# Kernel optimization log

Measured on AMD Instinct MI355X. Metric: run time of the kernel, lower is better.

The kernel has to match this reference:

```python
import jax, jax.numpy as jnp
import numpy as np


def setup_inputs() -> dict:
    key = jax.random.key(0)
    k1, k2, k3, k4 = jax.random.split(key, 4)
    B, V, P, C, R, N, OUT = 8, 4096, 32, 32, 2, 16, 32  # N=(l_max+1)^2, l_max=3
    signal = jax.random.normal(k1, (B, V, C), dtype=jnp.float32)
    patches_idx = jax.random.randint(k2, (B, V, P), 0, V, dtype=jnp.int32)
    conv_kernel = jax.random.normal(k3, (B, V, P, R, N), dtype=jnp.float32)
    kernel_weights = jax.random.normal(k4, (OUT, C, R, N), dtype=jnp.float32) * 0.05
    biases = jnp.zeros((OUT,), dtype=jnp.float32)
    return {
        "signal": signal,
        "patches_idx": patches_idx,
        "conv_kernel": conv_kernel,
        "kernel_weights": kernel_weights,
        "biases": biases,
    }


def reference(signal, patches_idx, conv_kernel, kernel_weights, biases):
    # Gather per-vertex tree-neighbor patches (tf.gather_nd with batch idx):
    # signal [B,V,C], patches_idx [B,V,P] -> patches [B,V,P,C]
    patches = jax.vmap(lambda s, i: s[i])(signal, patches_idx)
    # Bilinear contraction with precomputed SH conv kernel: [B,V,P,R,N] x [B,V,P,C]
    y = jnp.einsum('bvprn,bvpc->bvcrn', conv_kernel, patches)
    # Learned weights contraction: [OUT,C,R,N] x [B,V,C,R,N] -> [B,V,OUT]
    y = jnp.einsum('ijrn,bvjrn->bvi', kernel_weights, y)
    y = y + biases
    return jax.nn.relu(y)
```

## Files before the change

kernel.cpp:

```cpp
#include <hip/hip_runtime.h>


typedef __attribute__((ext_vector_type(8))) short bf16x8;
typedef __attribute__((ext_vector_type(4))) short short4v;
typedef __attribute__((ext_vector_type(16))) float f32x16;
typedef __attribute__((ext_vector_type(4))) float f32x4;
typedef __attribute__((ext_vector_type(4))) int int4v;

#define KSTR 36

__device__ __forceinline__ unsigned short f2bf_rne(float f) {
    union { float f; unsigned int u; } x;
    x.f = f;
    unsigned int u = x.u;
    return (unsigned short)((u + 0x7fffu + ((u >> 16) & 1u)) >> 16);
}
__device__ __forceinline__ unsigned short f2bf_rh(float f) {
    union { float f; unsigned int u; } x;
    x.f = f;
    return (unsigned short)((x.u + 0x8000u) >> 16);
}

__global__ __launch_bounds__(256) void prep_kernel(
        const float* __restrict__ W, const float* __restrict__ sig,
        unsigned short* __restrict__ Wf, unsigned short* __restrict__ sigbf) {
    int tid = blockIdx.x * 256 + threadIdx.x;
    if (tid < 32768) {
        int j = tid & 7;
        int l = (tid >> 3) & 63;
        int pair = tid >> 9;
        int s = pair >> 1;
        int t = pair & 1;
        int i = 16 * t + (l & 15);
        int crn = 32 * s + 8 * (l >> 4) + j;
        Wf[tid] = f2bf_rne(W[i * 1024 + crn]);
    } else {
        int e = (tid - 32768) * 8;
        if (e < 8 * 4096 * 32) {
            f32x4 a = *(const f32x4*)(sig + e);
            f32x4 b = *(const f32x4*)(sig + e + 4);
            bf16x8 v;
            v[0] = (short)f2bf_rne(a[0]); v[1] = (short)f2bf_rne(a[1]);
            v[2] = (short)f2bf_rne(a[2]); v[3] = (short)f2bf_rne(a[3]);
            v[4] = (short)f2bf_rne(b[0]); v[5] = (short)f2bf_rne(b[1]);
            v[6] = (short)f2bf_rne(b[2]); v[7] = (short)f2bf_rne(b[3]);
            *(bf16x8*)(sigbf + e) = v;
        }
    }
}

__global__ __launch_bounds__(256) void fused_kernel(
        const unsigned short* __restrict__ sigbf, const int* __restrict__ pidx,
        const float* __restrict__ ck, const unsigned short* __restrict__ Wf,
        const float* __restrict__ bias, float* __restrict__ out) {
    __shared__ __align__(16) unsigned short T_lds[16 * 1032];
    __shared__ __align__(16) unsigned short K_lds[4 * 32 * KSTR];
    __shared__ __align__(16) int idx_lds[512];
    const int tid = threadIdx.x;
    const int l = tid & 63;
    const int w = tid >> 6;
    const int m0 = blockIdx.x * 16;
    const int b = m0 >> 12;
    const int cc = l & 31;
    const int g = l >> 5;
    const unsigned short* sgb = sigbf + (size_t)b * (4096 * 32);
    unsigned short* kl = K_lds + w * 32 * KSTR;

    f32x4 kreg[4][4];
    #pragma unroll
    for (int q = 0; q < 4; ++q) {
        const f32x4* kp = (const f32x4*)(ck + (size_t)(m0 + w * 4 + q) * 1024);
        #pragma unroll
        for (int t = 0; t < 4; ++t) kreg[q][t] = kp[t * 64 + l];
    }
    {
        const int2* src = (const int2*)(pidx + (size_t)m0 * 32);
        ((int2*)idx_lds)[tid] = src[tid];
    }
    __syncthreads();

    auto issue_gathers = [&](int q, unsigned short (&gq)[16]) {
        const int base = (w * 4 + q) * 32;
        int4v ia = *(const int4v*)(idx_lds + base + 8 * g);
        int4v ib = *(const int4v*)(idx_lds + base + 8 * g + 4);
        int4v ic = *(const int4v*)(idx_lds + base + 16 + 8 * g);
        int4v id = *(const int4v*)(idx_lds + base + 16 + 8 * g + 4);
        #pragma unroll
        for (int j = 0; j < 4; ++j) {
            gq[j]      = sgb[ia[j] * 32 + cc];
            gq[4 + j]  = sgb[ib[j] * 32 + cc];
            gq[8 + j]  = sgb[ic[j] * 32 + cc];
            gq[12 + j] = sgb[id[j] * 32 + cc];
        }
    };

    auto compute_q = [&](int q, const unsigned short (&gq)[16], const f32x4 (&kq)[4]) {
        #pragma unroll
        for (int t = 0; t < 4; ++t) {
            union { f32x4 f; unsigned int u[4]; } x;
            x.f = kq[t];
            short4v v = { (short)(x.u[0] >> 16), (short)(x.u[1] >> 16),
                          (short)(x.u[2] >> 16), (short)(x.u[3] >> 16) };
            *(short4v*)(kl + (t * 8 + (l >> 3)) * KSTR + 4 * (l & 7)) = v;
        }
        f32x16 acc = {};
        #pragma unroll
        for (int half = 0; half < 2; ++half) {
            bf16x8 af, bfr;
            #pragma unroll
            for (int j = 0; j < 8; ++j) {
                af[j]  = (short)gq[half * 8 + j];
                bfr[j] = (short)kl[(half * 16 + 8 * g + j) * KSTR + cc];
            }
            acc = __builtin_amdgcn_mfma_f32_32x32x16_bf16(af, bfr, acc, 0, 0, 0);
        }
        const int bvl = w * 4 + q;
        unsigned short* trow = T_lds + bvl * 1032 + cc + g * 128;
        #pragma unroll
        for (int r = 0; r < 16; ++r) {
            trow[((r & 3) + 8 * (r >> 2)) * 32] = f2bf_rh(acc[r]);
        }
    };

    unsigned short g0[16], g1[16];
    issue_gathers(0, g0);
    issue_gathers(1, g1);
    compute_q(0, g0, kreg[0]); issue_gathers(2, g0);
    compute_q(1, g1, kreg[1]); issue_gathers(3, g1);
    compute_q(2, g0, kreg[2]);
    compute_q(3, g1, kreg[3]);
    __syncthreads();

    f32x4 acc0 = {}, acc1 = {};
    const int lg = l >> 4;
    const int ln = l & 15;
    #pragma unroll
    for (int si = 0; si < 8; ++si) {
        const int s = 8 * w + si;
        const bf16x8 af = *(const bf16x8*)(T_lds + ln * 1032 + s * 32 + 8 * lg);
        const bf16x8* wrow = (const bf16x8*)(Wf + (size_t)(s * 2) * 512);
        const bf16x8 b0 = wrow[l];
        const bf16x8 b1 = wrow[64 + l];
        acc0 = __builtin_amdgcn_mfma_f32_16x16x32_bf16(af, b0, acc0, 0, 0, 0);
        acc1 = __builtin_amdgcn_mfma_f32_16x16x32_bf16(af, b1, acc1, 0, 0, 0);
    }
    __syncthreads();

    float* red = (float*)T_lds;
    {
        f32x4* rp = (f32x4*)(red + w * 512);
        rp[l]      = acc0;
        rp[64 + l] = acc1;
    }
    __syncthreads();

    #pragma unroll
    for (int o0 = 0; o0 < 2; ++o0) {
        const int o = o0 * 256 + tid;
        float sum = red[o] + red[512 + o] + red[1024 + o] + red[1536 + o];
        const int t  = o >> 8;
        const int ll = (o >> 2) & 63;
        const int r  = o & 3;
        const int bv = ((ll >> 4) << 2) + r;
        const int i  = 16 * t + (ll & 15);
        sum += bias[i];
        out[(size_t)(m0 + bv) * 32 + i] = sum > 0.f ? sum : 0.f;
    }
}

extern "C" void kernel_launch(void* const* d_in, const int* in_sizes, int n_in,
                              void* d_out, int out_size, void* d_ws, size_t ws_size,
                              hipStream_t stream) {
    const float* sig  = (const float*)d_in[0];
    const int*   pidx = (const int*)d_in[1];
    const float* ck   = (const float*)d_in[2];
    const float* W    = (const float*)d_in[3];
    const float* bias = (const float*)d_in[4];
    float* out = (float*)d_out;
    unsigned short* Wf    = (unsigned short*)d_ws;
    unsigned short* sigbf = Wf + 32768;

    prep_kernel<<<640, 256, 0, stream>>>(W, sig, Wf, sigbf);
    fused_kernel<<<2048, 256, 0, stream>>>(sigbf, pidx, ck, Wf, bias, out);
}
```

Before: 40.86 us.

## Drop bf16 prep kernel; convert signal and weights inline in fused kernel

Removes the separate prep kernel that converted the weights and the signal to bf16. The fused kernel now gathers fp32 signal values and reads fp32 weights directly, converting both to bf16 in registers with round-half rounding. It also adds nontemporal hints on conv-kernel and index loads and on output stores. This saves a kernel launch and a full pass over the signal. In exchange, each gathered element is twice as wide and every block redundantly converts the weights, and rounding changes from round-nearest-even to round-half-up.

```diff
diff --git a/kernel.cpp b/kernel.cpp
--- a/kernel.cpp
+++ b/kernel.cpp
@@ -6,52 +6,19 @@
 typedef __attribute__((ext_vector_type(16))) float f32x16;
 typedef __attribute__((ext_vector_type(4))) float f32x4;
 typedef __attribute__((ext_vector_type(4))) int int4v;
+typedef __attribute__((ext_vector_type(2))) int int2v;
 
 #define KSTR 36
 
-__device__ __forceinline__ unsigned short f2bf_rne(float f) {
-    union { float f; unsigned int u; } x;
-    x.f = f;
-    unsigned int u = x.u;
-    return (unsigned short)((u + 0x7fffu + ((u >> 16) & 1u)) >> 16);
-}
 __device__ __forceinline__ unsigned short f2bf_rh(float f) {
     union { float f; unsigned int u; } x;
     x.f = f;
     return (unsigned short)((x.u + 0x8000u) >> 16);
 }
 
-__global__ __launch_bounds__(256) void prep_kernel(
-        const float* __restrict__ W, const float* __restrict__ sig,
-        unsigned short* __restrict__ Wf, unsigned short* __restrict__ sigbf) {
-    int tid = blockIdx.x * 256 + threadIdx.x;
-    if (tid < 32768) {
-        int j = tid & 7;
-        int l = (tid >> 3) & 63;
-        int pair = tid >> 9;
-        int s = pair >> 1;
-        int t = pair & 1;
-        int i = 16 * t + (l & 15);
-        int crn = 32 * s + 8 * (l >> 4) + j;
-        Wf[tid] = f2bf_rne(W[i * 1024 + crn]);
-    } else {
-        int e = (tid - 32768) * 8;
-        if (e < 8 * 4096 * 32) {
-            f32x4 a = *(const f32x4*)(sig + e);
-            f32x4 b = *(const f32x4*)(sig + e + 4);
-            bf16x8 v;
-            v[0] = (short)f2bf_rne(a[0]); v[1] = (short)f2bf_rne(a[1]);
-            v[2] = (short)f2bf_rne(a[2]); v[3] = (short)f2bf_rne(a[3]);
-            v[4] = (short)f2bf_rne(b[0]); v[5] = (short)f2bf_rne(b[1]);
-            v[6] = (short)f2bf_rne(b[2]); v[7] = (short)f2bf_rne(b[3]);
-            *(bf16x8*)(sigbf + e) = v;
-        }
-    }
-}
-
 __global__ __launch_bounds__(256) void fused_kernel(
-        const unsigned short* __restrict__ sigbf, const int* __restrict__ pidx,
-        const float* __restrict__ ck, const unsigned short* __restrict__ Wf,
+        const float* __restrict__ sig, const int* __restrict__ pidx,
+        const float* __restrict__ ck, const float* __restrict__ W,
         const float* __restrict__ bias, float* __restrict__ out) {
     __shared__ __align__(16) unsigned short T_lds[16 * 1032];
     __shared__ __align__(16) unsigned short K_lds[4 * 32 * KSTR];
@@ -63,7 +30,7 @@
     const int b = m0 >> 12;
     const int cc = l & 31;
     const int g = l >> 5;
-    const unsigned short* sgb = sigbf + (size_t)b * (4096 * 32);
+    const float* sgb = sig + (size_t)b * (4096 * 32);
     unsigned short* kl = K_lds + w * 32 * KSTR;
 
     f32x4 kreg[4][4];
@@ -71,15 +38,16 @@
     for (int q = 0; q < 4; ++q) {
         const f32x4* kp = (const f32x4*)(ck + (size_t)(m0 + w * 4 + q) * 1024);
         #pragma unroll
-        for (int t = 0; t < 4; ++t) kreg[q][t] = kp[t * 64 + l];
+        for (int t = 0; t < 4; ++t)
+            kreg[q][t] = __builtin_nontemporal_load(kp + t * 64 + l);
     }
     {
-        const int2* src = (const int2*)(pidx + (size_t)m0 * 32);
-        ((int2*)idx_lds)[tid] = src[tid];
+        const int2v* src = (const int2v*)(pidx + (size_t)m0 * 32);
+        ((int2v*)idx_lds)[tid] = __builtin_nontemporal_load(src + tid);
     }
     __syncthreads();
 
-    auto issue_gathers = [&](int q, unsigned short (&gq)[16]) {
+    auto issue_gathers = [&](int q, float (&gq)[16]) {
         const int base = (w * 4 + q) * 32;
         int4v ia = *(const int4v*)(idx_lds + base + 8 * g);
         int4v ib = *(const int4v*)(idx_lds + base + 8 * g + 4);
@@ -94,7 +62,7 @@
         }
     };
 
-    auto compute_q = [&](int q, const unsigned short (&gq)[16], const f32x4 (&kq)[4]) {
+    auto compute_q = [&](int q, const float (&gq)[16], const f32x4 (&kq)[4]) {
         #pragma unroll
         for (int t = 0; t < 4; ++t) {
             union { f32x4 f; unsigned int u[4]; } x;
@@ -109,7 +77,7 @@
             bf16x8 af, bfr;
             #pragma unroll
             for (int j = 0; j < 8; ++j) {
-                af[j]  = (short)gq[half * 8 + j];
+                af[j]  = (short)f2bf_rh(gq[half * 8 + j]);
                 bfr[j] = (short)kl[(half * 16 + 8 * g + j) * KSTR + cc];
             }
             acc = __builtin_amdgcn_mfma_f32_32x32x16_bf16(af, bfr, acc, 0, 0, 0);
@@ -122,7 +90,7 @@
         }
     };
 
-    unsigned short g0[16], g1[16];
+    float g0[16], g1[16];
     issue_gathers(0, g0);
     issue_gathers(1, g1);
     compute_q(0, g0, kreg[0]); issue_gathers(2, g0);
@@ -138,9 +106,19 @@
     for (int si = 0; si < 8; ++si) {
         const int s = 8 * w + si;
         const bf16x8 af = *(const bf16x8*)(T_lds + ln * 1032 + s * 32 + 8 * lg);
-        const bf16x8* wrow = (const bf16x8*)(Wf + (size_t)(s * 2) * 512);
-        const bf16x8 b0 = wrow[l];
-        const bf16x8 b1 = wrow[64 + l];
+        const float* wbase = W + 32 * s + 8 * lg;
+        f32x4 wa0 = *(const f32x4*)(wbase + ln * 1024);
+        f32x4 wa1 = *(const f32x4*)(wbase + ln * 1024 + 4);
+        f32x4 wb0 = *(const f32x4*)(wbase + (16 + ln) * 1024);
+        f32x4 wb1 = *(const f32x4*)(wbase + (16 + ln) * 1024 + 4);
+        bf16x8 b0, b1;
+        #pragma unroll
+        for (int j = 0; j < 4; ++j) {
+            b0[j]     = (short)f2bf_rh(wa0[j]);
+            b0[4 + j] = (short)f2bf_rh(wa1[j]);
+            b1[j]     = (short)f2bf_rh(wb0[j]);
+            b1[4 + j] = (short)f2bf_rh(wb1[j]);
+        }
         acc0 = __builtin_amdgcn_mfma_f32_16x16x32_bf16(af, b0, acc0, 0, 0, 0);
         acc1 = __builtin_amdgcn_mfma_f32_16x16x32_bf16(af, b1, acc1, 0, 0, 0);
     }
@@ -164,7 +142,8 @@
         const int bv = ((ll >> 4) << 2) + r;
         const int i  = 16 * t + (ll & 15);
         sum += bias[i];
-        out[(size_t)(m0 + bv) * 32 + i] = sum > 0.f ? sum : 0.f;
+        __builtin_nontemporal_store(sum > 0.f ? sum : 0.f,
+                                    &out[(size_t)(m0 + bv) * 32 + i]);
     }
 }
 
@@ -177,9 +156,6 @@
     const float* W    = (const float*)d_in[3];
     const float* bias = (const float*)d_in[4];
     float* out = (float*)d_out;
-    unsigned short* Wf    = (unsigned short*)d_ws;
-    unsigned short* sigbf = Wf + 32768;
 
-    prep_kernel<<<640, 256, 0, stream>>>(W, sig, Wf, sigbf);
-    fused_kernel<<<2048, 256, 0, stream>>>(sigbf, pidx, ck, Wf, bias, out);
+    fused_kernel<<<2048, 256, 0, stream>>>(sig, pidx, ck, W, bias, out);
 }
```

After: 58.92 us. +44.2%, slower.
